# Kernel optimization log

Measured on AMD Instinct MI355X. Metric: run time of the kernel, lower is better.

The kernel has to match this reference:

```python
import jax, jax.numpy as jnp
import numpy as np

N_E = 16384
SPLIT0, SPLIT1 = 64, 192
E_DIM = SPLIT0 + SPLIT1
BETA = 0.25
ENT_RATIO = 0.1
TEMP = 0.01
B, H, W = 4, 32, 32


def _l2norm(x, eps=1e-12):
    # matches F.normalize(p=2): x / max(||x||, eps)
    n = jnp.sqrt(jnp.sum(x * x, axis=-1, keepdims=True))
    return x / jnp.maximum(n, eps)


def _entropy_loss(affinity):
    a = affinity / TEMP  # [T, n_e]
    probs = jax.nn.softmax(a, axis=-1)
    log_probs = jax.nn.log_softmax(a + 1e-5, axis=-1)
    avg_probs = jnp.mean(probs, axis=0)
    avg_entropy = -jnp.sum(avg_probs * jnp.log(avg_probs + 1e-5))
    sample_entropy = -jnp.mean(jnp.sum(probs * log_probs, axis=-1))
    return sample_entropy - avg_entropy


def setup_inputs() -> dict:
    key = jax.random.key(0)
    k1, k2, k3 = jax.random.split(key, 3)
    z = jax.random.normal(k1, (B, E_DIM, H, W), dtype=jnp.float32)
    w_vqkd = jax.random.normal(k2, (N_E, SPLIT0), dtype=jnp.float32) / N_E
    w_vqgan = jax.random.normal(k3, (N_E, SPLIT1), dtype=jnp.float32) / N_E
    return {"z": z, "w_vqkd": w_vqkd, "w_vqgan": w_vqgan}


def reference(z, w_vqkd, w_vqgan):
    zb = jnp.transpose(z, (0, 2, 3, 1))            # [B,H,W,C]
    zf = zb.reshape(-1, E_DIM)                     # [T, C]
    zk = _l2norm(zf[:, :SPLIT0])                   # [T, d0]
    zg = _l2norm(zf[:, SPLIT0:])                   # [T, d1]
    ek = _l2norm(w_vqkd)                           # [n_e, d0]
    eg = _l2norm(w_vqgan)                          # [n_e, d1]
    z_norm = jnp.concatenate([zk, zg], axis=-1)    # [T, C]

    # ||z||^2 + ||e||^2 - 2 z.e  for each sub-codebook
    d_k = (jnp.sum(zk * zk, axis=1, keepdims=True)
           + jnp.sum(ek * ek, axis=1)
           - 2.0 * jnp.einsum('td,nd->tn', zk, ek))  # [T, n_e]
    d_g = (jnp.sum(zg * zg, axis=1, keepdims=True)
           + jnp.sum(eg * eg, axis=1)
           - 2.0 * jnp.einsum('td,nd->tn', zg, eg))  # [T, n_e]

    vqkd_d_norm = jnp.mean(jnp.sum(d_k ** 2, axis=-1))
    vqgan_d_norm = jnp.mean(jnp.sum(d_g ** 2, axis=-1))

    d = d_k + d_g
    idx = jnp.argmin(d, axis=1)                    # [T]

    all_emb = jnp.concatenate([ek, eg], axis=-1)   # [n_e, C]
    z_q_flat = all_emb[idx]                        # gather [T, C]
    z_q = z_q_flat.reshape(zb.shape)
    z_cont = z_norm.reshape(zb.shape)

    vq_loss = jnp.mean((z_q - jax.lax.stop_gradient(z_cont)) ** 2)
    commit_loss = BETA * jnp.mean((jax.lax.stop_gradient(z_q) - z_cont) ** 2)
    entropy_loss = ENT_RATIO * _entropy_loss(-d)

    # straight-through estimator
    z_q_st = z_cont + jax.lax.stop_gradient(z_q - z_cont)
    z_q_out = jnp.transpose(z_q_st, (0, 3, 1, 2))  # back to NCHW
    return (z_q_out, vq_loss, commit_loss, entropy_loss,
            vqkd_d_norm, vqgan_d_norm, idx)
```

## Files before the change

### kernel.cpp

```cpp
#include <hip/hip_runtime.h>


#define T_TOK 4096
#define NE    16384
#define KD    256
#define KE    256
#define CAP   1024
#define DCUT  0.13f
#define RTHR  0.004f

#define NCB   512
#define NZB   128
#define NGRAM 282
#define NGEMM 4096

typedef __attribute__((ext_vector_type(8))) short bf16x8;
typedef __attribute__((ext_vector_type(4))) float f32x4;
typedef unsigned long long u64;

__device__ __forceinline__ short f2bf(float f) {
    unsigned u = __float_as_uint(f);
    u = (u + 0x7FFFu + ((u >> 16) & 1u)) >> 16;
    return (short)u;
}
__device__ __forceinline__ float bf2f(short s) {
    return __uint_as_float(((unsigned)(unsigned short)s) << 16);
}

__device__ __forceinline__ void async_load16(const void* g, void* l) {
    __builtin_amdgcn_global_load_lds(
        (const __attribute__((address_space(1))) void*)g,
        (__attribute__((address_space(3))) void*)l, 16, 0, 0);
}

__global__ __launch_bounds__(256)
void megaprep_kernel(const float* __restrict__ wk, const float* __restrict__ wg,
                     const float* __restrict__ z,
                     float* __restrict__ enorm, float* __restrict__ e2k,
                     float* __restrict__ e2s, short* __restrict__ Es,
                     float* __restrict__ znorm, float* __restrict__ z2k,
                     float* __restrict__ z2s, short* __restrict__ Zs,
                     float* __restrict__ SVeS, float* __restrict__ SVeV,
                     float* __restrict__ SVzS, float* __restrict__ SVzV,
                     float* __restrict__ mompart,
                     u64* __restrict__ packed, float* __restrict__ avg_num,
                     int* __restrict__ ncand, float* __restrict__ scal,
                     float* __restrict__ G, int* __restrict__ done_ctr) {
    int b = blockIdx.x, tid = threadIdx.x;
    if (b >= NCB + NZB) {
        int gid = (b - NCB - NZB) * 256 + tid;
        for (int i = gid; i < 81920; i += 2048) G[i] = 0.f;
        for (int i = gid; i < NE; i += 2048) avg_num[i] = 0.f;
        for (int i = gid; i < T_TOK; i += 2048) { packed[i] = ~0ull; ncand[i] = 0; }
        if (gid < 8) scal[gid] = 0.f;
        if (gid == 8) *done_ctr = 0;
        return;
    }

    __shared__ float xs[32][257];
    __shared__ float ps[32][8];
    __shared__ float rnorm[32][2];
    __shared__ float rw[32][2];

    if (b < NCB) {
        int n0 = b * 32;
#pragma unroll
        for (int i = 0; i < 8; ++i) {
            int idx = tid + i * 256;
            xs[idx >> 6][idx & 63] = wk[(size_t)n0 * 64 + idx];
        }
#pragma unroll
        for (int i = 0; i < 24; ++i) {
            int idx = tid + i * 256;
            xs[idx / 192][64 + idx % 192] = wg[(size_t)n0 * 192 + idx];
        }
        __syncthreads();
        {
            int r = tid & 31, part = tid >> 5;
            float s = 0.f;
            for (int j = 0; j < 32; ++j) { float v = xs[r][part * 32 + j]; s = fmaf(v, v, s); }
            ps[r][part] = s;
        }
        __syncthreads();
        if (tid < 32) {
            float sk = ps[tid][0] + ps[tid][1];
            float sg = ps[tid][2] + ps[tid][3] + ps[tid][4] + ps[tid][5] + ps[tid][6] + ps[tid][7];
            float nk = fmaxf(sqrtf(sk), 1e-12f), ng = fmaxf(sqrtf(sg), 1e-12f);
            float ek2 = sk / (nk * nk), eg2 = sg / (ng * ng);
            rnorm[tid][0] = 1.f / nk; rnorm[tid][1] = 1.f / ng;
            rw[tid][0] = ek2; rw[tid][1] = eg2;
            e2k[n0 + tid] = ek2; e2s[n0 + tid] = ek2 + eg2;
        }
        __syncthreads();
        int c = tid;
        for (int i = 0; i < 32; ++i) {
            float y = xs[i][c] * rnorm[i][(c < 64) ? 0 : 1];
            enorm[(size_t)(n0 + i) * KD + c] = y;
            Es[(size_t)(n0 + i) * KE + c] = f2bf(-2.f * y);
        }
        {
            int sel = (c < 64) ? 0 : 1;
            float S = 0.f, V = 0.f;
            for (int r = 0; r < 32; ++r) {
                float y = xs[r][c] * rnorm[r][sel];
                S += y; V = fmaf(rw[r][sel], y, V);
            }
            SVeS[(size_t)b * 256 + c] = S;
            SVeV[(size_t)b * 256 + c] = V;
        }
        if (tid < 32) {
            float a = rw[tid][0], g = rw[tid][1];
            float s0 = a, s1 = a * a, s2 = g, s3 = g * g;
#pragma unroll
            for (int m = 1; m < 32; m <<= 1) {
                s0 += __shfl_xor(s0, m, 64); s1 += __shfl_xor(s1, m, 64);
                s2 += __shfl_xor(s2, m, 64); s3 += __shfl_xor(s3, m, 64);
            }
            if (tid == 0) {
                mompart[b * 4 + 0] = s0; mompart[b * 4 + 1] = s1;
                mompart[b * 4 + 2] = s2; mompart[b * 4 + 3] = s3;
            }
        }
    } else {
        int jz = b - NCB;
        int t0 = jz * 32;
        int bb = t0 >> 10, hw0 = t0 & 1023;
#pragma unroll
        for (int i = 0; i < 32; ++i) {
            int idx = tid + i * 256;
            int cc = idx >> 5, hwl = idx & 31;
            xs[hwl][cc] = z[(((size_t)bb * 256 + cc) << 10) + hw0 + hwl];
        }
        __syncthreads();
        {
            int r = tid & 31, part = tid >> 5;
            float s = 0.f;
            for (int j = 0; j < 32; ++j) { float v = xs[r][part * 32 + j]; s = fmaf(v, v, s); }
            ps[r][part] = s;
        }
        __syncthreads();
        if (tid < 32) {
            float sk = ps[tid][0] + ps[tid][1];
            float sg = ps[tid][2] + ps[tid][3] + ps[tid][4] + ps[tid][5] + ps[tid][6] + ps[tid][7];
            float nk = fmaxf(sqrtf(sk), 1e-12f), ng = fmaxf(sqrtf(sg), 1e-12f);
            float zk2 = sk / (nk * nk), zg2 = sg / (ng * ng);
            rnorm[tid][0] = 1.f / nk; rnorm[tid][1] = 1.f / ng;
            rw[tid][0] = zk2; rw[tid][1] = zg2;
            z2k[t0 + tid] = zk2; z2s[t0 + tid] = zk2 + zg2;
        }
        __syncthreads();
        int c = tid;
        for (int i = 0; i < 32; ++i) {
            float y = xs[i][c] * rnorm[i][(c < 64) ? 0 : 1];
            znorm[(size_t)(t0 + i) * KD + c] = y;
            Zs[(size_t)(t0 + i) * KE + c] = f2bf(y);
        }
        {
            int sel = (c < 64) ? 0 : 1;
            float S = 0.f, V = 0.f;
            for (int r = 0; r < 32; ++r) {
                float y = xs[r][c] * rnorm[r][sel];
                S += y; V = fmaf(rw[r][sel], y, V);
            }
            SVzS[(size_t)jz * 256 + c] = S;
            SVzV[(size_t)jz * 256 + c] = V;
        }
        if (tid < 32) {
            float a = rw[tid][0], g = rw[tid][1];
            float s0 = a, s1 = a * a, s2 = g, s3 = g * g;
#pragma unroll
            for (int m = 1; m < 32; m <<= 1) {
                s0 += __shfl_xor(s0, m, 64); s1 += __shfl_xor(s1, m, 64);
                s2 += __shfl_xor(s2, m, 64); s3 += __shfl_xor(s3, m, 64);
            }
            if (tid == 0) {
                mompart[b * 4 + 0] = s0; mompart[b * 4 + 1] = s1;
                mompart[b * 4 + 2] = s2; mompart[b * 4 + 3] = s3;
            }
        }
    }
}

template <int W>
__device__ __forceinline__ void gram_strip(const float* __restrict__ X, float* __restrict__ G,
                                           int i0s, int r0, int rows, int c0,
                                           float* xs, int tid) {
    const int JW = W / 32;
    int ia = tid >> 5;
    int jb = tid & 31;
    float acc[4][JW];
#pragma unroll
    for (int a = 0; a < 4; ++a)
#pragma unroll
        for (int u = 0; u < JW; ++u) acc[a][u] = 0.f;
    for (int rb = 0; rb < rows; rb += 16) {
        __syncthreads();
        for (int lin = tid; lin < 4 * W; lin += 256) {
            int r = lin / (W / 4), f4 = lin % (W / 4);
            *(float4*)&xs[r * W + f4 * 4] =
                *(const float4*)&X[(size_t)(r0 + rb + r) * KD + c0 + f4 * 4];
        }
        __syncthreads();
#pragma unroll 4
        for (int r = 0; r < 16; ++r) {
            float4 xi = *(const float4*)&xs[r * W + i0s + ia * 4];
            float xj[JW];
#pragma unroll
            for (int u = 0; u < JW; ++u) xj[u] = xs[r * W + jb * JW + u];
#pragma unroll
            for (int a = 0; a < 4; ++a)
#pragma unroll
                for (int u = 0; u < JW; ++u)
                    acc[a][u] = fmaf(xi[a], xj[u], acc[a][u]);
        }
    }
#pragma unroll
    for (int a = 0; a < 4; ++a) {
        int i = i0s + ia * 4 + a;
#pragma unroll
        for (int u = 0; u < JW; ++u)
            atomicAdd(&G[i * W + jb * JW + u], acc[a][u]);
    }
}

__global__ __launch_bounds__(256, 4)
void gemm_gram_kernel(const short* __restrict__ Zs, const short* __restrict__ Es,
                      const float* __restrict__ z2s, const float* __restrict__ e2s,
                      u64* __restrict__ packed,
                      float* __restrict__ candD, int* __restrict__ candN,
                      int* __restrict__ ncand,
                      const float* __restrict__ znorm, const float* __restrict__ enorm,
                      float* __restrict__ Gbuf,
                      const float* __restrict__ SVeS, const float* __restrict__ SVeV,
                      const float* __restrict__ SVzS, const float* __restrict__ SVzV,
                      const float* __restrict__ mompart,
                      float* __restrict__ SV, float* __restrict__ mom) {
    __shared__ __align__(16) char smem[32768];
    const int gid = blockIdx.x, tid = threadIdx.x;

    if (gid < NGRAM) {
        int b = gid;
        float* xs = (float*)smem;
        float* r1 = (float*)(smem + 12288);
        float* r2 = (float*)(smem + 13312);

        if (b == 280) {
            int c = tid;
            float s = 0.f, v = 0.f;
            for (int j = 0; j < NZB; ++j) { s += SVzS[(size_t)j * 256 + c]; v += SVzV[(size_t)j * 256 + c]; }
            SV[c] = s; SV[256 + c] = v;
            s = 0.f; v = 0.f;
            for (int j = 0; j < NCB; ++j) { s += SVeS[(size_t)j * 256 + c]; v += SVeV[(size_t)j * 256 + c]; }
            SV[512 + c] = s; SV[768 + c] = v;
            return;
        }
        if (b == 281) {
            int q = tid & 3, grp = tid >> 2;
            float accE = 0.f, accZ = 0.f;
            for (int j = grp; j < NCB; j += 64) accE += mompart[j * 4 + q];
            for (int j = NCB + grp; j < NCB + NZB; j += 64) accZ += mompart[j * 4 + q];
            r1[tid] = accE; r2[tid] = accZ;
            __syncthreads();
            for (int st = 32; st > 0; st >>= 1) {
                if (grp < st) { r1[tid] += r1[tid + st * 4]; r2[tid] += r2[tid + st * 4]; }
                __syncthreads();
            }
            if (grp == 0) { mom[4 + q] = r1[q]; mom[q] = r2[q]; }
            return;
        }
        if (b < 192) {
            gram_strip<192>(enorm, Gbuf + 4096, (b >> 5) * 32, (b & 31) * 512, 512, 64, xs, tid);
        } else if (b < 224) {
            int l = b - 192;
            gram_strip<64>(enorm, Gbuf, (l >> 4) * 32, (l & 15) * 1024, 1024, 0, xs, tid);
        } else if (b < 272) {
            int l = b - 224;
            gram_strip<192>(znorm, Gbuf + 45056, (l >> 3) * 32, (l & 7) * 512, 512, 64, xs, tid);
        } else {
            int l = b - 272;
            gram_strip<64>(znorm, Gbuf + 40960, (l >> 2) * 32, (l & 3) * 1024, 1024, 0, xs, tid);
        }
        return;
    }

    short* As = (short*)smem;
    short* Bs = As + 128 * 64;
    const int g = gid - NGRAM;
    const int lane = tid & 63, wid = tid >> 6;
    const int wm = wid >> 1, wn = wid & 1;
    const int t0 = (g & 31) * 128, n0 = (g >> 5) * 128;

    f32x4 acc[4][4];
#pragma unroll
    for (int bi = 0; bi < 4; ++bi)
#pragma unroll
        for (int bj = 0; bj < 4; ++bj) {
            f32x4 zz = {0.f, 0.f, 0.f, 0.f};
            acc[bi][bj] = zz;
        }

    auto stage = [&](int k0) {
        const int rb0 = wid * 32;
#pragma unroll
        for (int c2 = 0; c2 < 4; ++c2) {
            int rb = rb0 + c2 * 8;
            int row = rb + (lane >> 3);
            int q = (lane & 7) ^ (lane >> 3);
            async_load16(Zs + (size_t)(t0 + row) * KE + k0 + q * 8, &As[rb * 64]);
            async_load16(Es + (size_t)(n0 + row) * KE + k0 + q * 8, &Bs[rb * 64]);
        }
    };
    auto compute_half = [&](int s) {
        bf16x8 bfv[4];
#pragma unroll
        for (int bj = 0; bj < 4; ++bj) {
            int brow = wn * 64 + bj * 16 + (lane & 15);
            int q = ((s << 2) | (lane >> 4)) ^ (brow & 7);
            bfv[bj] = *reinterpret_cast<const bf16x8*>(&Bs[brow * 64 + q * 8]);
        }
#pragma unroll
        for (int bi = 0; bi < 4; ++bi) {
            int arow = wm * 64 + bi * 16 + (lane & 15);
            int q = ((s << 2) | (lane >> 4)) ^ (arow & 7);
            bf16x8 af = *reinterpret_cast<const bf16x8*>(&As[arow * 64 + q * 8]);
#pragma unroll
            for (int bj = 0; bj < 4; ++bj)
                acc[bi][bj] = __builtin_amdgcn_mfma_f32_16x16x32_bf16(
                    af, bfv[bj], acc[bi][bj], 0, 0, 0);
        }
    };

    int k0 = 0;
    for (int r = 0; r < 4; ++r) {
        stage(k0); __syncthreads();
        compute_half(0); compute_half(1);
        __syncthreads(); k0 += 64;
    }

    u64*   tokmin = (u64*)smem;
    float* bthr   = (float*)(smem + 2048);

    float e2sv[4];
#pragma unroll
    for (int bj = 0; bj < 4; ++bj)
        e2sv[bj] = e2s[n0 + wn * 64 + bj * 16 + (lane & 15)];

#pragma unroll
    for (int bi = 0; bi < 4; ++bi) {
        u64 pmin[4] = {~0ull, ~0ull, ~0ull, ~0ull};
        f32x4 z4 = *reinterpret_cast<const f32x4*>(
            &z2s[t0 + wm * 64 + bi * 16 + (lane >> 4) * 4]);
#pragma unroll
        for (int reg = 0; reg < 4; ++reg) {
#pragma unroll
            for (int bj = 0; bj < 4; ++bj) {
                float d = z4[reg] + e2sv[bj] + acc[bi][bj][reg];
                int n = n0 + wn * 64 + bj * 16 + (lane & 15);
                u64 pv = (((u64)__float_as_uint(d)) << 32) | (unsigned)n;
                if (pv < pmin[reg]) pmin[reg] = pv;
            }
        }
#pragma unroll
        for (int m = 1; m < 16; m <<= 1)
#pragma unroll
            for (int reg = 0; reg < 4; ++reg) {
                u64 o = __shfl_xor(pmin[reg], m, 64);
                if (o < pmin[reg]) pmin[reg] = o;
            }
        if ((lane & 15) == 0) {
#pragma unroll
            for (int reg = 0; reg < 4; ++reg) {
                int tl = wm * 64 + bi * 16 + (lane >> 4) * 4 + reg;
                tokmin[tl * 2 + wn] = pmin[reg];
            }
        }
    }
    __syncthreads();

    if (tid < 128) {
        int tl = tid;
        u64 bm = tokmin[tl * 2], b1 = tokmin[tl * 2 + 1];
        if (b1 < bm) bm = b1;
        u64 old = atomicMin(&packed[t0 + tl], bm);
        u64 gb = (old < bm) ? old : bm;
        bthr[tl] = __uint_as_float((unsigned)(gb >> 32)) + DCUT;
    }
    __syncthreads();

#pragma unroll
    for (int bi = 0; bi < 4; ++bi) {
        f32x4 z4 = *reinterpret_cast<const f32x4*>(
            &z2s[t0 + wm * 64 + bi * 16 + (lane >> 4) * 4]);
#pragma unroll
        for (int reg = 0; reg < 4; ++reg) {
            int tl = wm * 64 + bi * 16 + (lane >> 4) * 4 + reg;
            int t = t0 + tl;
            float thr = bthr[tl];
#pragma unroll
            for (int bj = 0; bj < 4; ++bj) {
                float d = z4[reg] + e2sv[bj] + acc[bi][bj][reg];
                bool hit = (d <= thr);
                u64 mask = __ballot(hit);
                unsigned gm = (unsigned)((mask >> ((lane >> 4) << 4)) & 0xFFFFu);
                int cnt = __popc(gm);
                if (cnt) {
                    int pos0 = 0;
                    if ((lane & 15) == 0) pos0 = atomicAdd(&ncand[t], cnt);
                    pos0 = __shfl(pos0, (lane >> 4) << 4, 64);
                    if (hit) {
                        int pos = pos0 + __popc(gm & ((1u << (lane & 15)) - 1u));
                        if (pos < CAP) {
                            candD[(size_t)t * CAP + pos] = d;
                            candN[(size_t)t * CAP + pos] = n0 + wn * 64 + bj * 16 + (lane & 15);
                        }
                    }
                }
            }
        }
    }
}

__global__ __launch_bounds__(256)
void combine_final_kernel(const u64* __restrict__ packed,
                          const float* __restrict__ enorm, const float* __restrict__ znorm,
                          const float* __restrict__ z2s, const float* __restrict__ e2s,
                          float* __restrict__ candD, const int* __restrict__ candN,
                          const int* __restrict__ ncand, float* __restrict__ avg_num,
                          float* __restrict__ scal, int* __restrict__ done_ctr,
                          const float* __restrict__ G, const float* __restrict__ SV,
                          const float* __restrict__ mom, float* __restrict__ out) {
    __shared__ float Zts[16], entp[16];
    __shared__ int idxs[16];
    __shared__ float q_lds[256][17];
    __shared__ float red[256];
    __shared__ int lastf;
    int tid = threadIdx.x;
    int tbase = blockIdx.x * 16;

    {
        int tok = tid >> 4, sub = tid & 15;
        int tt = tbase + tok;
        u64 pv = packed[tt];
        float dmin = __uint_as_float((unsigned)(pv >> 32));
        float M = -100.f * dmin;
        int nc = min(ncand[tt], CAP);
        size_t base = (size_t)tt * CAP;
        float Zp = 0.f, Wp = 0.f;
        float bestd = 1e30f; int bestn = (int)(pv & 0xFFFFFFFFull);
        for (int i = sub; i < nc; i += 16) {
            float dap = candD[base + i];
            float a = -100.f * dap;
            float e = __expf(a - M);
            candD[base + i] = e;
            Zp += e; Wp = fmaf(a, e, Wp);
            if (dap <= dmin + RTHR) {
                int n = candN[base + i];
                const float4* ep = (const float4*)&enorm[(size_t)n * KD];
                const float4* zp = (const float4*)&znorm[(size_t)tt * KD];
                float s0 = 0.f, s1 = 0.f, s2 = 0.f, s3 = 0.f;
                for (int j = 0; j < 64; ++j) {
                    float4 ev = ep[j], zv = zp[j];
                    s0 = fmaf(ev.x, zv.x, s0); s1 = fmaf(ev.y, zv.y, s1);
                    s2 = fmaf(ev.z, zv.z, s2); s3 = fmaf(ev.w, zv.w, s3);
                }
                float dex = z2s[tt] + e2s[n] - 2.f * ((s0 + s1) + (s2 + s3));
                if (dex < bestd) { bestd = dex; bestn = n; }
            }
        }
        u64 pb = (((u64)__float_as_uint(bestd)) << 32) | (unsigned)bestn;
#pragma unroll
        for (int m = 1; m < 16; m <<= 1) {
            Zp += __shfl_xor(Zp, m, 64);
            Wp += __shfl_xor(Wp, m, 64);
            u64 o = __shfl_xor(pb, m, 64);
            if (o < pb) pb = o;
        }
        if (sub == 0) {
            Zts[tok] = Zp;
            int idx = (int)(pb & 0xFFFFFFFFull);
            idxs[tok] = idx;
            out[1048581 + tt] = (float)idx;
            entp[tok] = M + logf(Zp) - Wp / Zp;
        }
    }
    __syncthreads();
    if (tid == 0) {
        float ent = 0.f;
#pragma unroll
        for (int i = 0; i < 16; ++i) ent += entp[i];
        atomicAdd(&scal[3], ent);
    }

    float sdq = 0.f;
    for (int tl2 = 0; tl2 < 16; ++tl2) {
        int tt = tbase + tl2;
        float qv = enorm[(size_t)idxs[tl2] * KD + tid];
        q_lds[tid][tl2] = qv;
        float zc = znorm[(size_t)tt * KD + tid];
        float df = qv - zc;
        sdq = fmaf(df, df, sdq);
    }
    __syncthreads();
    {
        int bb = tbase >> 10, hw0 = tbase & 1023;
        int cg = tid >> 4, hwl = tid & 15;
        for (int c0 = 0; c0 < 256; c0 += 16) {
            int c = c0 + cg;
            out[(((size_t)(bb * 256 + c)) << 10) + hw0 + hwl] = q_lds[c][hwl];
        }
    }
    red[tid] = sdq;
    __syncthreads();
    for (int s = 128; s > 0; s >>= 1) { if (tid < s) red[tid] += red[tid + s]; __syncthreads(); }
    if (tid == 0) atomicAdd(&scal[2], red[0]);

    {
        int tok = tid >> 4, sub = tid & 15;
        int tt = tbase + tok;
        int nc = min(ncand[tt], CAP);
        float rZ = 1.f / Zts[tok];
        for (int i = sub; i < nc; i += 16) {
            atomicAdd(&avg_num[candN[(size_t)tt * CAP + i]],
                      candD[(size_t)tt * CAP + i] * rZ);
        }
    }

    __syncthreads();
    __threadfence();
    if (tid == 0) lastf = (atomicAdd(done_ctr, 1) == 255) ? 1 : 0;
    __syncthreads();
    if (!lastf) return;
    __threadfence();

    float s = 0.f;
#pragma unroll 4
    for (int n = tid; n < NE; n += 256) {
        float avg = atomicAdd(&avg_num[n], 0.f) * (1.f / 4096.f);
        s += avg * logf(avg + 1e-5f);
    }
    red[tid] = s; __syncthreads();
    for (int st = 128; st > 0; st >>= 1) { if (tid < st) red[tid] += red[tid + st]; __syncthreads(); }
    float avg_ent_neg = red[0];
    __syncthreads();

    const float* G_ek = G;
    const float* G_eg = G + 4096;
    const float* G_zk = G + 40960;
    const float* G_zg = G + 45056;
    float rk = 0.f, rg = 0.f;
#pragma unroll 4
    for (int i = tid; i < 4096; i += 256)  rk = fmaf(G_zk[i], G_ek[i], rk);
#pragma unroll 4
    for (int i = tid; i < 36864; i += 256) rg = fmaf(G_zg[i], G_eg[i], rg);
    {
        int c = tid;
        float v = SV[256 + c] * SV[512 + c] + SV[c] * SV[768 + c];
        if (c < 64) rk -= v; else rg -= v;
    }
    red[tid] = 4.f * rk; __syncthreads();
    for (int st = 128; st > 0; st >>= 1) { if (tid < st) red[tid] += red[tid + st]; __syncthreads(); }
    float red_k = red[0];
    __syncthreads();
    red[tid] = 4.f * rg; __syncthreads();
    for (int st = 128; st > 0; st >>= 1) { if (tid < st) red[tid] += red[tid + st]; __syncthreads(); }
    float red_g = red[0];

    if (tid == 0) {
        float term1k = NE * mom[1] + 2.f * mom[0] * mom[4] + T_TOK * mom[5];
        float term1g = NE * mom[3] + 2.f * mom[2] * mom[6] + T_TOK * mom[7];
        float sdk2 = term1k + red_k;
        float sdg2 = term1g + red_g;
        float avg_ent = -avg_ent_neg;
        float se = atomicAdd(&scal[3], 0.f) * (1.f / 4096.f);
        float vq = atomicAdd(&scal[2], 0.f) * (1.f / 1048576.f);
        out[1048576] = vq;
        out[1048577] = 0.25f * vq;
        out[1048578] = 0.1f * (se - avg_ent);
        out[1048579] = sdk2 * (1.f / 4096.f);
        out[1048580] = sdg2 * (1.f / 4096.f);
    }
}

extern "C" void kernel_launch(void* const* d_in, const int* in_sizes, int n_in,
                              void* d_out, int out_size, void* d_ws, size_t ws_size,
                              hipStream_t stream) {
    const float* z  = (const float*)d_in[0];
    const float* wk = (const float*)d_in[1];
    const float* wg = (const float*)d_in[2];
    float* out = (float*)d_out;

    char* ws = (char*)d_ws;
    size_t off = 0;
    auto alloc = [&](size_t bytes) {
        void* p = ws + off;
        off += (bytes + 255) & ~(size_t)255;
        return p;
    };
    float* enorm  = (float*)alloc((size_t)NE * KD * 4);
    float* znorm  = (float*)alloc((size_t)T_TOK * KD * 4);
    short* Es     = (short*)alloc((size_t)NE * KE * 2);
    short* Zs     = (short*)alloc((size_t)T_TOK * KE * 2);
    float* e2k    = (float*)alloc(NE * 4);
    float* e2s    = (float*)alloc(NE * 4);
    float* z2k    = (float*)alloc(T_TOK * 4);
    float* z2s    = (float*)alloc(T_TOK * 4);
    u64*   packed = (u64*)alloc(T_TOK * 8);
    int*   ncand  = (int*)alloc(T_TOK * 4);
    float* candD  = (float*)alloc((size_t)T_TOK * CAP * 4);
    int*   candN  = (int*)alloc((size_t)T_TOK * CAP * 4);
    float* avg_num= (float*)alloc(NE * 4);
    float* scal   = (float*)alloc(8 * 4);
    float* Gbuf   = (float*)alloc(81920 * 4);
    float* SV     = (float*)alloc(1024 * 4);
    float* momv   = (float*)alloc(8 * 4);
    float* SVeS   = (float*)alloc((size_t)NCB * 256 * 4);
    float* SVeV   = (float*)alloc((size_t)NCB * 256 * 4);
    float* SVzS   = (float*)alloc((size_t)NZB * 256 * 4);
    float* SVzV   = (float*)alloc((size_t)NZB * 256 * 4);
    float* mompart= (float*)alloc((size_t)(NCB + NZB) * 4 * 4);
    int*   done_ctr = (int*)alloc(256);

    megaprep_kernel<<<NCB + NZB + 8, 256, 0, stream>>>(
        wk, wg, z, enorm, e2k, e2s, Es, znorm, z2k, z2s, Zs,
        SVeS, SVeV, SVzS, SVzV, mompart, packed, avg_num, ncand, scal, Gbuf, done_ctr);

    gemm_gram_kernel<<<NGRAM + NGEMM, 256, 0, stream>>>(
        Zs, Es, z2s, e2s, packed,
        candD, candN, ncand, znorm, enorm, Gbuf,
        SVeS, SVeV, SVzS, SVzV, mompart, SV, momv);

    combine_final_kernel<<<256, 256, 0, stream>>>(
        packed, enorm, znorm, z2s, e2s,
        candD, candN, ncand, avg_num, scal, done_ctr, Gbuf, SV, momv, out);
}
```

Before: 283.7 us.

## Move Gram-matrix and reduction blocks from GEMM kernel into combine kernel

Moves the 282 Gram-strip, SV-reduction and moment-reduction blocks out of the GEMM launch and into the combine/final launch, next to the 256 per-token combine blocks. The GEMM kernel becomes a pure 4096-block MFMA distance kernel. The Gram work now runs alongside the combine work, and the last-block counter is updated to cover all 538 blocks. This removes the Gram blocks' tail interference from the heavy GEMM, but the combine launch gets longer and its shared memory is reused for the Gram scratch buffers.

```diff
diff --git a/kernel.cpp b/kernel.cpp
--- a/kernel.cpp
+++ b/kernel.cpp
@@ -13,6 +13,7 @@
 #define NZB   128
 #define NGRAM 282
 #define NGEMM 4096
+#define NCOMB 256
 
 typedef __attribute__((ext_vector_type(8))) short bf16x8;
 typedef __attribute__((ext_vector_type(4))) float f32x4;
@@ -224,68 +225,17 @@
 }
 
 __global__ __launch_bounds__(256, 4)
-void gemm_gram_kernel(const short* __restrict__ Zs, const short* __restrict__ Es,
-                      const float* __restrict__ z2s, const float* __restrict__ e2s,
-                      u64* __restrict__ packed,
-                      float* __restrict__ candD, int* __restrict__ candN,
-                      int* __restrict__ ncand,
-                      const float* __restrict__ znorm, const float* __restrict__ enorm,
-                      float* __restrict__ Gbuf,
-                      const float* __restrict__ SVeS, const float* __restrict__ SVeV,
-                      const float* __restrict__ SVzS, const float* __restrict__ SVzV,
-                      const float* __restrict__ mompart,
-                      float* __restrict__ SV, float* __restrict__ mom) {
+void gemm_kernel(const short* __restrict__ Zs, const short* __restrict__ Es,
+                 const float* __restrict__ z2s, const float* __restrict__ e2s,
+                 u64* __restrict__ packed,
+                 float* __restrict__ candD, int* __restrict__ candN,
+                 int* __restrict__ ncand) {
     __shared__ __align__(16) char smem[32768];
-    const int gid = blockIdx.x, tid = threadIdx.x;
-
-    if (gid < NGRAM) {
-        int b = gid;
-        float* xs = (float*)smem;
-        float* r1 = (float*)(smem + 12288);
-        float* r2 = (float*)(smem + 13312);
-
-        if (b == 280) {
-            int c = tid;
-            float s = 0.f, v = 0.f;
-            for (int j = 0; j < NZB; ++j) { s += SVzS[(size_t)j * 256 + c]; v += SVzV[(size_t)j * 256 + c]; }
-            SV[c] = s; SV[256 + c] = v;
-            s = 0.f; v = 0.f;
-            for (int j = 0; j < NCB; ++j) { s += SVeS[(size_t)j * 256 + c]; v += SVeV[(size_t)j * 256 + c]; }
-            SV[512 + c] = s; SV[768 + c] = v;
-            return;
-        }
-        if (b == 281) {
-            int q = tid & 3, grp = tid >> 2;
-            float accE = 0.f, accZ = 0.f;
-            for (int j = grp; j < NCB; j += 64) accE += mompart[j * 4 + q];
-            for (int j = NCB + grp; j < NCB + NZB; j += 64) accZ += mompart[j * 4 + q];
-            r1[tid] = accE; r2[tid] = accZ;
-            __syncthreads();
-            for (int st = 32; st > 0; st >>= 1) {
-                if (grp < st) { r1[tid] += r1[tid + st * 4]; r2[tid] += r2[tid + st * 4]; }
-                __syncthreads();
-            }
-            if (grp == 0) { mom[4 + q] = r1[q]; mom[q] = r2[q]; }
-            return;
-        }
-        if (b < 192) {
-            gram_strip<192>(enorm, Gbuf + 4096, (b >> 5) * 32, (b & 31) * 512, 512, 64, xs, tid);
-        } else if (b < 224) {
-            int l = b - 192;
-            gram_strip<64>(enorm, Gbuf, (l >> 4) * 32, (l & 15) * 1024, 1024, 0, xs, tid);
-        } else if (b < 272) {
-            int l = b - 224;
-            gram_strip<192>(znorm, Gbuf + 45056, (l >> 3) * 32, (l & 7) * 512, 512, 64, xs, tid);
-        } else {
-            int l = b - 272;
-            gram_strip<64>(znorm, Gbuf + 40960, (l >> 2) * 32, (l & 3) * 1024, 1024, 0, xs, tid);
-        }
-        return;
-    }
+    const int tid = threadIdx.x;
 
     short* As = (short*)smem;
     short* Bs = As + 128 * 64;
-    const int g = gid - NGRAM;
+    const int g = blockIdx.x;
     const int lane = tid & 63, wid = tid >> 6;
     const int wm = wid >> 1, wn = wid & 1;
     const int t0 = (g & 31) * 128, n0 = (g >> 5) * 128;
@@ -427,107 +377,153 @@
                           float* __restrict__ candD, const int* __restrict__ candN,
                           const int* __restrict__ ncand, float* __restrict__ avg_num,
                           float* __restrict__ scal, int* __restrict__ done_ctr,
-                          const float* __restrict__ G, const float* __restrict__ SV,
-                          const float* __restrict__ mom, float* __restrict__ out) {
+                          float* __restrict__ G, float* __restrict__ SV,
+                          float* __restrict__ mom,
+                          const float* __restrict__ SVeS, const float* __restrict__ SVeV,
+                          const float* __restrict__ SVzS, const float* __restrict__ SVzV,
+                          const float* __restrict__ mompart,
+                          float* __restrict__ out) {
+    __shared__ __align__(16) float q_lds[256][17];
+    __shared__ float red[256];
     __shared__ float Zts[16], entp[16];
     __shared__ int idxs[16];
-    __shared__ float q_lds[256][17];
-    __shared__ float red[256];
     __shared__ int lastf;
     int tid = threadIdx.x;
-    int tbase = blockIdx.x * 16;
-
-    {
-        int tok = tid >> 4, sub = tid & 15;
-        int tt = tbase + tok;
-        u64 pv = packed[tt];
-        float dmin = __uint_as_float((unsigned)(pv >> 32));
-        float M = -100.f * dmin;
-        int nc = min(ncand[tt], CAP);
-        size_t base = (size_t)tt * CAP;
-        float Zp = 0.f, Wp = 0.f;
-        float bestd = 1e30f; int bestn = (int)(pv & 0xFFFFFFFFull);
-        for (int i = sub; i < nc; i += 16) {
-            float dap = candD[base + i];
-            float a = -100.f * dap;
-            float e = __expf(a - M);
-            candD[base + i] = e;
-            Zp += e; Wp = fmaf(a, e, Wp);
-            if (dap <= dmin + RTHR) {
-                int n = candN[base + i];
-                const float4* ep = (const float4*)&enorm[(size_t)n * KD];
-                const float4* zp = (const float4*)&znorm[(size_t)tt * KD];
-                float s0 = 0.f, s1 = 0.f, s2 = 0.f, s3 = 0.f;
-                for (int j = 0; j < 64; ++j) {
-                    float4 ev = ep[j], zv = zp[j];
-                    s0 = fmaf(ev.x, zv.x, s0); s1 = fmaf(ev.y, zv.y, s1);
-                    s2 = fmaf(ev.z, zv.z, s2); s3 = fmaf(ev.w, zv.w, s3);
+    int bid = blockIdx.x;
+
+    if (bid < NGRAM) {
+        int b = bid;
+        float* xs = (float*)q_lds;
+        float* r1 = red;
+        float* r2 = (float*)q_lds;
+
+        if (b == 280) {
+            int c = tid;
+            float s = 0.f, v = 0.f;
+            for (int j = 0; j < NZB; ++j) { s += SVzS[(size_t)j * 256 + c]; v += SVzV[(size_t)j * 256 + c]; }
+            SV[c] = s; SV[256 + c] = v;
+            s = 0.f; v = 0.f;
+            for (int j = 0; j < NCB; ++j) { s += SVeS[(size_t)j * 256 + c]; v += SVeV[(size_t)j * 256 + c]; }
+            SV[512 + c] = s; SV[768 + c] = v;
+        } else if (b == 281) {
+            int q = tid & 3, grp = tid >> 2;
+            float accE = 0.f, accZ = 0.f;
+            for (int j = grp; j < NCB; j += 64) accE += mompart[j * 4 + q];
+            for (int j = NCB + grp; j < NCB + NZB; j += 64) accZ += mompart[j * 4 + q];
+            r1[tid] = accE; r2[tid] = accZ;
+            __syncthreads();
+            for (int st = 32; st > 0; st >>= 1) {
+                if (grp < st) { r1[tid] += r1[tid + st * 4]; r2[tid] += r2[tid + st * 4]; }
+                __syncthreads();
+            }
+            if (grp == 0) { mom[4 + q] = r1[q]; mom[q] = r2[q]; }
+        } else if (b < 192) {
+            gram_strip<192>(enorm, G + 4096, (b >> 5) * 32, (b & 31) * 512, 512, 64, xs, tid);
+        } else if (b < 224) {
+            int l = b - 192;
+            gram_strip<64>(enorm, G, (l >> 4) * 32, (l & 15) * 1024, 1024, 0, xs, tid);
+        } else if (b < 272) {
+            int l = b - 224;
+            gram_strip<192>(znorm, G + 45056, (l >> 3) * 32, (l & 7) * 512, 512, 64, xs, tid);
+        } else {
+            int l = b - 272;
+            gram_strip<64>(znorm, G + 40960, (l >> 2) * 32, (l & 3) * 1024, 1024, 0, xs, tid);
+        }
+    } else {
+        int tbase = (bid - NGRAM) * 16;
+
+        {
+            int tok = tid >> 4, sub = tid & 15;
+            int tt = tbase + tok;
+            u64 pv = packed[tt];
+            float dmin = __uint_as_float((unsigned)(pv >> 32));
+            float M = -100.f * dmin;
+            int nc = min(ncand[tt], CAP);
+            size_t base = (size_t)tt * CAP;
+            float Zp = 0.f, Wp = 0.f;
+            float bestd = 1e30f; int bestn = (int)(pv & 0xFFFFFFFFull);
+            for (int i = sub; i < nc; i += 16) {
+                float dap = candD[base + i];
+                float a = -100.f * dap;
+                float e = __expf(a - M);
+                candD[base + i] = e;
+                Zp += e; Wp = fmaf(a, e, Wp);
+                if (dap <= dmin + RTHR) {
+                    int n = candN[base + i];
+                    const float4* ep = (const float4*)&enorm[(size_t)n * KD];
+                    const float4* zp = (const float4*)&znorm[(size_t)tt * KD];
+                    float s0 = 0.f, s1 = 0.f, s2 = 0.f, s3 = 0.f;
+                    for (int j = 0; j < 64; ++j) {
+                        float4 ev = ep[j], zv = zp[j];
+                        s0 = fmaf(ev.x, zv.x, s0); s1 = fmaf(ev.y, zv.y, s1);
+                        s2 = fmaf(ev.z, zv.z, s2); s3 = fmaf(ev.w, zv.w, s3);
+                    }
+                    float dex = z2s[tt] + e2s[n] - 2.f * ((s0 + s1) + (s2 + s3));
+                    if (dex < bestd) { bestd = dex; bestn = n; }
                 }
-                float dex = z2s[tt] + e2s[n] - 2.f * ((s0 + s1) + (s2 + s3));
-                if (dex < bestd) { bestd = dex; bestn = n; }
-            }
-        }
-        u64 pb = (((u64)__float_as_uint(bestd)) << 32) | (unsigned)bestn;
-#pragma unroll
-        for (int m = 1; m < 16; m <<= 1) {
-            Zp += __shfl_xor(Zp, m, 64);
-            Wp += __shfl_xor(Wp, m, 64);
-            u64 o = __shfl_xor(pb, m, 64);
-            if (o < pb) pb = o;
-        }
-        if (sub == 0) {
-            Zts[tok] = Zp;
-            int idx = (int)(pb & 0xFFFFFFFFull);
-            idxs[tok] = idx;
-            out[1048581 + tt] = (float)idx;
-            entp[tok] = M + logf(Zp) - Wp / Zp;
-        }
-    }
-    __syncthreads();
-    if (tid == 0) {
-        float ent = 0.f;
-#pragma unroll
-        for (int i = 0; i < 16; ++i) ent += entp[i];
-        atomicAdd(&scal[3], ent);
-    }
-
-    float sdq = 0.f;
-    for (int tl2 = 0; tl2 < 16; ++tl2) {
-        int tt = tbase + tl2;
-        float qv = enorm[(size_t)idxs[tl2] * KD + tid];
-        q_lds[tid][tl2] = qv;
-        float zc = znorm[(size_t)tt * KD + tid];
-        float df = qv - zc;
-        sdq = fmaf(df, df, sdq);
-    }
-    __syncthreads();
-    {
-        int bb = tbase >> 10, hw0 = tbase & 1023;
-        int cg = tid >> 4, hwl = tid & 15;
-        for (int c0 = 0; c0 < 256; c0 += 16) {
-            int c = c0 + cg;
-            out[(((size_t)(bb * 256 + c)) << 10) + hw0 + hwl] = q_lds[c][hwl];
-        }
-    }
-    red[tid] = sdq;
-    __syncthreads();
-    for (int s = 128; s > 0; s >>= 1) { if (tid < s) red[tid] += red[tid + s]; __syncthreads(); }
-    if (tid == 0) atomicAdd(&scal[2], red[0]);
-
-    {
-        int tok = tid >> 4, sub = tid & 15;
-        int tt = tbase + tok;
-        int nc = min(ncand[tt], CAP);
-        float rZ = 1.f / Zts[tok];
-        for (int i = sub; i < nc; i += 16) {
-            atomicAdd(&avg_num[candN[(size_t)tt * CAP + i]],
-                      candD[(size_t)tt * CAP + i] * rZ);
+            }
+            u64 pb = (((u64)__float_as_uint(bestd)) << 32) | (unsigned)bestn;
+#pragma unroll
+            for (int m = 1; m < 16; m <<= 1) {
+                Zp += __shfl_xor(Zp, m, 64);
+                Wp += __shfl_xor(Wp, m, 64);
+                u64 o = __shfl_xor(pb, m, 64);
+                if (o < pb) pb = o;
+            }
+            if (sub == 0) {
+                Zts[tok] = Zp;
+                int idx = (int)(pb & 0xFFFFFFFFull);
+                idxs[tok] = idx;
+                out[1048581 + tt] = (float)idx;
+                entp[tok] = M + logf(Zp) - Wp / Zp;
+            }
+        }
+        __syncthreads();
+        if (tid == 0) {
+            float ent = 0.f;
+#pragma unroll
+            for (int i = 0; i < 16; ++i) ent += entp[i];
+            atomicAdd(&scal[3], ent);
+        }
+
+        float sdq = 0.f;
+        for (int tl2 = 0; tl2 < 16; ++tl2) {
+            int tt = tbase + tl2;
+            float qv = enorm[(size_t)idxs[tl2] * KD + tid];
+            q_lds[tid][tl2] = qv;
+            float zc = znorm[(size_t)tt * KD + tid];
+            float df = qv - zc;
+            sdq = fmaf(df, df, sdq);
+        }
+        __syncthreads();
+        {
+            int bb = tbase >> 10, hw0 = tbase & 1023;
+            int cg = tid >> 4, hwl = tid & 15;
+            for (int c0 = 0; c0 < 256; c0 += 16) {
+                int c = c0 + cg;
+                out[(((size_t)(bb * 256 + c)) << 10) + hw0 + hwl] = q_lds[c][hwl];
+            }
+        }
+        red[tid] = sdq;
+        __syncthreads();
+        for (int s = 128; s > 0; s >>= 1) { if (tid < s) red[tid] += red[tid + s]; __syncthreads(); }
+        if (tid == 0) atomicAdd(&scal[2], red[0]);
+
+        {
+            int tok = tid >> 4, sub = tid & 15;
+            int tt = tbase + tok;
+            int nc = min(ncand[tt], CAP);
+            float rZ = 1.f / Zts[tok];
+            for (int i = sub; i < nc; i += 16) {
+                atomicAdd(&avg_num[candN[(size_t)tt * CAP + i]],
+                          candD[(size_t)tt * CAP + i] * rZ);
+            }
         }
     }
 
     __syncthreads();
     __threadfence();
-    if (tid == 0) lastf = (atomicAdd(done_ctr, 1) == 255) ? 1 : 0;
+    if (tid == 0) lastf = (atomicAdd(done_ctr, 1) == (NGRAM + NCOMB - 1)) ? 1 : 0;
     __syncthreads();
     if (!lastf) return;
     __threadfence();
@@ -624,12 +620,11 @@
         wk, wg, z, enorm, e2k, e2s, Es, znorm, z2k, z2s, Zs,
         SVeS, SVeV, SVzS, SVzV, mompart, packed, avg_num, ncand, scal, Gbuf, done_ctr);
 
-    gemm_gram_kernel<<<NGRAM + NGEMM, 256, 0, stream>>>(
-        Zs, Es, z2s, e2s, packed,
-        candD, candN, ncand, znorm, enorm, Gbuf,
-        SVeS, SVeV, SVzS, SVzV, mompart, SV, momv);
-
-    combine_final_kernel<<<256, 256, 0, stream>>>(
+    gemm_kernel<<<NGEMM, 256, 0, stream>>>(
+        Zs, Es, z2s, e2s, packed, candD, candN, ncand);
+
+    combine_final_kernel<<<NGRAM + NCOMB, 256, 0, stream>>>(
         packed, enorm, znorm, z2s, e2s,
-        candD, candN, ncand, avg_num, scal, done_ctr, Gbuf, SV, momv, out);
-}
+        candD, candN, ncand, avg_num, scal, done_ctr,
+        Gbuf, SV, momv, SVeS, SVeV, SVzS, SVzV, mompart, out);
+}
```

Result: slower. 320.4 us (+12.9%).
